# Optimization experiments

Measured on AMD Instinct MI355X. Metric: run time of the kernel, lower is better.

## Reference

```python
import jax, jax.numpy as jnp
import numpy as np

BATCH = 4096
DIM = 512
TEMP = 0.1

def setup_inputs() -> dict:
    key = jax.random.key(0)
    k1, k2 = jax.random.split(key)
    emb_i = jax.random.normal(k1, (BATCH, DIM), dtype=jnp.float32)
    emb_j = jax.random.normal(k2, (BATCH, DIM), dtype=jnp.float32)
    return {"emb_i": emb_i, "emb_j": emb_j}

def _l2_normalize(x, eps=1e-12):
    # matches torch F.normalize(dim=1): x / max(||x||, eps)
    norm = jnp.sqrt(jnp.sum(x * x, axis=1, keepdims=True))
    return x / jnp.maximum(norm, eps)

def reference(emb_i, emb_j):
    n = emb_i.shape[0]
    z_i = _l2_normalize(emb_i)
    z_j = _l2_normalize(emb_j)
    reps = jnp.concatenate([z_i, z_j], axis=0)  # [2N, D], rows unit-norm
    # cosine similarity of unit vectors == dot product -> GEMM instead of O(N^2 D) broadcast
    sim = reps @ reps.T  # [2N, 2N]
    # positives: diag offsets +N and -N
    pos_ij = jnp.sum(z_i * z_j, axis=1)  # diag(sim, +N)
    pos_ji = pos_ij                      # diag(sim, -N) is identical by symmetry
    positives = jnp.concatenate([pos_ij, pos_ji], axis=0)  # [2N]
    nominator = jnp.exp(positives / TEMP)
    neg_mask = 1.0 - jnp.eye(2 * n, dtype=sim.dtype)
    denominator = jnp.sum(neg_mask * jnp.exp(sim / TEMP), axis=1)  # [2N]
    loss_partial = -jnp.log(nominator / denominator)
    return jnp.sum(loss_partial) / (2 * n)
```

## Files before the change

### kernel.cpp

```cpp
#include <hip/hip_runtime.h>
#include <hip/hip_bf16.h>

#define N_ROWS 4096
#define DIM    512
#define M_ROWS 8192
#define BK     32
#define EXP_SCALE 14.4269504088896340736f

typedef unsigned short ushort_t;
typedef __attribute__((ext_vector_type(8))) short short8;
typedef __attribute__((ext_vector_type(4))) float f32x4;

__device__ __forceinline__ ushort_t f2bf(float x) {
  unsigned int bits = __float_as_uint(x);
  unsigned int lsb = (bits >> 16) & 1u;
  bits += 0x7fffu + lsb;
  return (ushort_t)(bits >> 16);
}

__device__ __forceinline__ void store4bf(ushort_t* p, float4 v, float s) {
  union { ushort_t u[4]; uint2 d; } pk;
  pk.u[0] = f2bf(v.x * s);
  pk.u[1] = f2bf(v.y * s);
  pk.u[2] = f2bf(v.z * s);
  pk.u[3] = f2bf(v.w * s);
  *(uint2*)p = pk.d;
}

__device__ __forceinline__ void async16(const ushort_t* g, ushort_t* l) {
  __builtin_amdgcn_global_load_lds(
      (const __attribute__((address_space(1))) void*)g,
      (__attribute__((address_space(3))) void*)l,
      16, 0, 0);
}

__global__ __launch_bounds__(64) void norm_kernel(
    const float* __restrict__ ei, const float* __restrict__ ej,
    ushort_t* __restrict__ reps, float* __restrict__ pos) {
  int b = blockIdx.x;
  int lane = threadIdx.x;
  const float4* pi = (const float4*)(ei + (size_t)b * DIM);
  const float4* pj = (const float4*)(ej + (size_t)b * DIM);
  float4 a0 = pi[lane];
  float4 a1 = pi[lane + 64];
  float4 b0 = pj[lane];
  float4 b1 = pj[lane + 64];

  float si = a0.x*a0.x + a0.y*a0.y + a0.z*a0.z + a0.w*a0.w
           + a1.x*a1.x + a1.y*a1.y + a1.z*a1.z + a1.w*a1.w;
  float sj = b0.x*b0.x + b0.y*b0.y + b0.z*b0.z + b0.w*b0.w
           + b1.x*b1.x + b1.y*b1.y + b1.z*b1.z + b1.w*b1.w;
  float dp = a0.x*b0.x + a0.y*b0.y + a0.z*b0.z + a0.w*b0.w
           + a1.x*b1.x + a1.y*b1.y + a1.z*b1.z + a1.w*b1.w;

#pragma unroll
  for (int m = 32; m >= 1; m >>= 1) {
    si += __shfl_xor(si, m, 64);
    sj += __shfl_xor(sj, m, 64);
    dp += __shfl_xor(dp, m, 64);
  }
  float ii = 1.0f / fmaxf(sqrtf(si), 1e-12f);
  float ij = 1.0f / fmaxf(sqrtf(sj), 1e-12f);
  if (lane == 0) pos[b] = dp * ii * ij;

  ushort_t* ri = reps + (size_t)b * DIM;
  ushort_t* rj = reps + (size_t)(b + N_ROWS) * DIM;
  store4bf(ri + lane * 4,       a0, ii);
  store4bf(ri + 256 + lane * 4, a1, ii);
  store4bf(rj + lane * 4,       b0, ij);
  store4bf(rj + 256 + lane * 4, b1, ij);
}

__global__ __launch_bounds__(256) void sim_kernel(
    const ushort_t* __restrict__ reps, float* __restrict__ denom) {
  int bj = blockIdx.x, bi = blockIdx.y;
  if (bi > bj) return;

  __shared__ ushort_t As[128 * BK];
  __shared__ ushort_t Bs[128 * BK];

  int tid  = threadIdx.x;
  int wave = tid >> 6, lane = tid & 63;
  int wr = wave >> 1, wc = wave & 1;
  int quad = lane >> 4, l15 = lane & 15;

  int c0 = wave * 2, c1 = c0 + 1;
  int srow  = lane >> 2;
  int selem = (lane & 3) * 8;
  const ushort_t* gA0 = reps + (size_t)(bi * 128 + c0 * 16 + srow) * DIM + selem;
  const ushort_t* gA1 = reps + (size_t)(bi * 128 + c1 * 16 + srow) * DIM + selem;
  const ushort_t* gB0 = reps + (size_t)(bj * 128 + c0 * 16 + srow) * DIM + selem;
  const ushort_t* gB1 = reps + (size_t)(bj * 128 + c1 * 16 + srow) * DIM + selem;
  ushort_t* lA0 = As + c0 * 512;
  ushort_t* lA1 = As + c1 * 512;
  ushort_t* lB0 = Bs + c0 * 512;
  ushort_t* lB1 = Bs + c1 * 512;

  f32x4 zero4 = {0.0f, 0.0f, 0.0f, 0.0f};
  f32x4 acc[4][4];
#pragma unroll
  for (int tr = 0; tr < 4; ++tr)
#pragma unroll
    for (int tc = 0; tc < 4; ++tc) acc[tr][tc] = zero4;

  for (int kk = 0; kk < DIM; kk += BK) {
    __syncthreads();
    async16(gA0 + kk, lA0);
    async16(gA1 + kk, lA1);
    async16(gB0 + kk, lB0);
    async16(gB1 + kk, lB1);
    __syncthreads();

    short8 aF[4], bF[4];
#pragma unroll
    for (int t = 0; t < 4; ++t) {
      aF[t] = *(const short8*)(As + (wr * 64 + t * 16 + l15) * BK + quad * 8);
      bF[t] = *(const short8*)(Bs + (wc * 64 + t * 16 + l15) * BK + quad * 8);
    }
#pragma unroll
    for (int tr = 0; tr < 4; ++tr)
#pragma unroll
      for (int tc = 0; tc < 4; ++tc)
        acc[tr][tc] = __builtin_amdgcn_mfma_f32_16x16x32_bf16(
            aF[tr], bF[tc], acc[tr][tc], 0, 0, 0);
  }

  int rowg_base = bi * 128 + wr * 64;
  int colg_base = bj * 128 + wc * 64;

  f32x4 rsum[4];
  float csum[4] = {0.0f, 0.0f, 0.0f, 0.0f};
#pragma unroll
  for (int tr = 0; tr < 4; ++tr) rsum[tr] = zero4;

#pragma unroll
  for (int tr = 0; tr < 4; ++tr) {
    int rowg0 = rowg_base + tr * 16 + quad * 4;
#pragma unroll
    for (int tc = 0; tc < 4; ++tc) {
      int colg = colg_base + tc * 16 + l15;
      f32x4 a = acc[tr][tc];
      f32x4 e;
#pragma unroll
      for (int r = 0; r < 4; ++r) {
        float v = exp2f(a[r] * EXP_SCALE);
        e[r] = ((rowg0 + r) == colg) ? 0.0f : v;
      }
      rsum[tr] += e;
      csum[tc] += e[0] + e[1] + e[2] + e[3];
    }
  }

#pragma unroll
  for (int m = 1; m <= 8; m <<= 1)
#pragma unroll
    for (int tr = 0; tr < 4; ++tr)
#pragma unroll
      for (int r = 0; r < 4; ++r)
        rsum[tr][r] += __shfl_xor(rsum[tr][r], m, 64);

  if (l15 == 0) {
#pragma unroll
    for (int tr = 0; tr < 4; ++tr)
#pragma unroll
      for (int r = 0; r < 4; ++r)
        atomicAdd(&denom[rowg_base + tr * 16 + quad * 4 + r], rsum[tr][r]);
  }

  if (bi != bj) {
#pragma unroll
    for (int m = 16; m <= 32; m <<= 1)
#pragma unroll
      for (int tc = 0; tc < 4; ++tc)
        csum[tc] += __shfl_xor(csum[tc], m, 64);
    if (quad == 0) {
#pragma unroll
      for (int tc = 0; tc < 4; ++tc)
        atomicAdd(&denom[colg_base + tc * 16 + l15], csum[tc]);
    }
  }
}

__global__ __launch_bounds__(256) void loss_kernel(
    const float* __restrict__ denom, const float* __restrict__ pos,
    float* __restrict__ out) {
  __shared__ float red[4];
  int tid = threadIdx.x;
  float p = 0.0f;
  for (int r = tid; r < M_ROWS; r += 256)
    p += logf(denom[r]) - pos[r & (N_ROWS - 1)] * 10.0f;
#pragma unroll
  for (int m = 32; m >= 1; m >>= 1) p += __shfl_xor(p, m, 64);
  if ((tid & 63) == 0) red[tid >> 6] = p;
  __syncthreads();
  if (tid == 0)
    out[0] = (red[0] + red[1] + red[2] + red[3]) * (1.0f / M_ROWS);
}

extern "C" void kernel_launch(void* const* d_in, const int* in_sizes, int n_in,
                              void* d_out, int out_size, void* d_ws, size_t ws_size,
                              hipStream_t stream) {
  const float* ei = (const float*)d_in[0];
  const float* ej = (const float*)d_in[1];
  float* out = (float*)d_out;

  char* ws = (char*)d_ws;
  ushort_t* reps = (ushort_t*)ws;
  float* denom = (float*)(ws + (size_t)M_ROWS * DIM * 2);
  float* pos = (float*)(ws + (size_t)M_ROWS * DIM * 2 + M_ROWS * 4);

  hipMemsetAsync(denom, 0, M_ROWS * sizeof(float), stream);
  norm_kernel<<<N_ROWS, 64, 0, stream>>>(ei, ej, reps, pos);
  sim_kernel<<<dim3(64, 64), 256, 0, stream>>>(reps, denom);
  loss_kernel<<<1, 256, 0, stream>>>(denom, pos, out);
}
```

Baseline: 156.6 us.

## Double-buffer sim kernel LDS tiles, swizzle LDS, launch only upper-triangle blocks

The similarity GEMM now double-buffers its A/B LDS tiles. It issues the async global-to-LDS loads for the next K-slice before computing the current one, which removes one barrier per iteration and overlaps loads with MFMA work. LDS chunks are XOR-swizzled on write and read to reduce bank conflicts. The grid launches exactly the 2080 upper-triangle tiles, with an index decode in place of half the blocks exiting early. The norm and loss kernels also get larger blocks, at the cost of doubled LDS use per sim block and a little index arithmetic.

Result: slower. 164.1 us (+4.8%).

```diff
diff --git a/kernel.cpp b/kernel.cpp
--- a/kernel.cpp
+++ b/kernel.cpp
@@ -5,6 +5,8 @@
 #define DIM    512
 #define M_ROWS 8192
 #define BK     32
+#define NITER  (DIM / BK)
+#define TILE_E (128 * BK)
 #define EXP_SCALE 14.4269504088896340736f
 
 typedef unsigned short ushort_t;
@@ -34,11 +36,11 @@
       16, 0, 0);
 }
 
-__global__ __launch_bounds__(64) void norm_kernel(
+__global__ __launch_bounds__(256) void norm_kernel(
     const float* __restrict__ ei, const float* __restrict__ ej,
     ushort_t* __restrict__ reps, float* __restrict__ pos) {
-  int b = blockIdx.x;
-  int lane = threadIdx.x;
+  int b = blockIdx.x * 4 + (threadIdx.x >> 6);
+  int lane = threadIdx.x & 63;
   const float4* pi = (const float4*)(ei + (size_t)b * DIM);
   const float4* pj = (const float4*)(ej + (size_t)b * DIM);
   float4 a0 = pi[lane];
@@ -73,11 +75,14 @@
 
 __global__ __launch_bounds__(256) void sim_kernel(
     const ushort_t* __restrict__ reps, float* __restrict__ denom) {
-  int bj = blockIdx.x, bi = blockIdx.y;
-  if (bi > bj) return;
-
-  __shared__ ushort_t As[128 * BK];
-  __shared__ ushort_t Bs[128 * BK];
+  int t = blockIdx.x;
+  int bi = (int)((129.0f - sqrtf((float)(16641 - 8 * t))) * 0.5f);
+  while (bi * (129 - bi) / 2 > t) --bi;
+  while ((bi + 1) * (128 - bi) / 2 <= t) ++bi;
+  int bj = bi + (t - bi * (129 - bi) / 2);
+
+  __shared__ ushort_t As[2][TILE_E];
+  __shared__ ushort_t Bs[2][TILE_E];
 
   int tid  = threadIdx.x;
   int wave = tid >> 6, lane = tid & 63;
@@ -86,15 +91,12 @@
 
   int c0 = wave * 2, c1 = c0 + 1;
   int srow  = lane >> 2;
-  int selem = (lane & 3) * 8;
+  int selem = (((lane & 3) ^ (srow & 3)) * 8);
   const ushort_t* gA0 = reps + (size_t)(bi * 128 + c0 * 16 + srow) * DIM + selem;
   const ushort_t* gA1 = reps + (size_t)(bi * 128 + c1 * 16 + srow) * DIM + selem;
   const ushort_t* gB0 = reps + (size_t)(bj * 128 + c0 * 16 + srow) * DIM + selem;
   const ushort_t* gB1 = reps + (size_t)(bj * 128 + c1 * 16 + srow) * DIM + selem;
-  ushort_t* lA0 = As + c0 * 512;
-  ushort_t* lA1 = As + c1 * 512;
-  ushort_t* lB0 = Bs + c0 * 512;
-  ushort_t* lB1 = Bs + c1 * 512;
+  int c0o = c0 * 512, c1o = c1 * 512;
 
   f32x4 zero4 = {0.0f, 0.0f, 0.0f, 0.0f};
   f32x4 acc[4][4];
@@ -103,19 +105,29 @@
 #pragma unroll
     for (int tc = 0; tc < 4; ++tc) acc[tr][tc] = zero4;
 
-  for (int kk = 0; kk < DIM; kk += BK) {
+  int sw = (quad ^ (l15 & 3)) * 8;
+
+  async16(gA0, &As[0][c0o]);
+  async16(gA1, &As[0][c1o]);
+  async16(gB0, &Bs[0][c0o]);
+  async16(gB1, &Bs[0][c1o]);
+
+  for (int k = 0; k < NITER; ++k) {
     __syncthreads();
-    async16(gA0 + kk, lA0);
-    async16(gA1 + kk, lA1);
-    async16(gB0 + kk, lB0);
-    async16(gB1 + kk, lB1);
-    __syncthreads();
-
+    if (k + 1 < NITER) {
+      int off = (k + 1) * BK;
+      int nb = (k + 1) & 1;
+      async16(gA0 + off, &As[nb][c0o]);
+      async16(gA1 + off, &As[nb][c1o]);
+      async16(gB0 + off, &Bs[nb][c0o]);
+      async16(gB1 + off, &Bs[nb][c1o]);
+    }
+    int cb = k & 1;
     short8 aF[4], bF[4];
 #pragma unroll
-    for (int t = 0; t < 4; ++t) {
-      aF[t] = *(const short8*)(As + (wr * 64 + t * 16 + l15) * BK + quad * 8);
-      bF[t] = *(const short8*)(Bs + (wc * 64 + t * 16 + l15) * BK + quad * 8);
+    for (int tt = 0; tt < 4; ++tt) {
+      aF[tt] = *(const short8*)(&As[cb][(wr * 64 + tt * 16 + l15) * BK + sw]);
+      bF[tt] = *(const short8*)(&Bs[cb][(wc * 64 + tt * 16 + l15) * BK + sw]);
     }
 #pragma unroll
     for (int tr = 0; tr < 4; ++tr)
@@ -181,20 +193,24 @@
   }
 }
 
-__global__ __launch_bounds__(256) void loss_kernel(
+__global__ __launch_bounds__(1024) void loss_kernel(
     const float* __restrict__ denom, const float* __restrict__ pos,
     float* __restrict__ out) {
-  __shared__ float red[4];
+  __shared__ float red[16];
   int tid = threadIdx.x;
   float p = 0.0f;
-  for (int r = tid; r < M_ROWS; r += 256)
+  for (int r = tid; r < M_ROWS; r += 1024)
     p += logf(denom[r]) - pos[r & (N_ROWS - 1)] * 10.0f;
 #pragma unroll
   for (int m = 32; m >= 1; m >>= 1) p += __shfl_xor(p, m, 64);
   if ((tid & 63) == 0) red[tid >> 6] = p;
   __syncthreads();
-  if (tid == 0)
-    out[0] = (red[0] + red[1] + red[2] + red[3]) * (1.0f / M_ROWS);
+  if (tid == 0) {
+    float s = 0.0f;
+#pragma unroll
+    for (int w = 0; w < 16; ++w) s += red[w];
+    out[0] = s * (1.0f / M_ROWS);
+  }
 }
 
 extern "C" void kernel_launch(void* const* d_in, const int* in_sizes, int n_in,
@@ -210,7 +226,7 @@
   float* pos = (float*)(ws + (size_t)M_ROWS * DIM * 2 + M_ROWS * 4);
 
   hipMemsetAsync(denom, 0, M_ROWS * sizeof(float), stream);
-  norm_kernel<<<N_ROWS, 64, 0, stream>>>(ei, ej, reps, pos);
-  sim_kernel<<<dim3(64, 64), 256, 0, stream>>>(reps, denom);
-  loss_kernel<<<1, 256, 0, stream>>>(denom, pos, out);
-}
+  norm_kernel<<<N_ROWS / 4, 256, 0, stream>>>(ei, ej, reps, pos);
+  sim_kernel<<<2080, 256, 0, stream>>>(reps, denom);
+  loss_kernel<<<1, 1024, 0, stream>>>(denom, pos, out);
+}
```
